# Optimization experiments

Hardware: AMD Instinct MI355X
Metric: run time of the kernel (lower is better)

## Reference

```python
import jax, jax.numpy as jnp
import numpy as np

B, T, I, H = 64, 512, 1024, 1024


def setup_inputs() -> dict:
    key = jax.random.key(0)
    ks = jax.random.split(key, 7)
    s = 1.0 / np.sqrt(H)  # PyTorch GRUCell init range
    return {
        "input": jax.random.normal(ks[0], (B, T, I), jnp.float32),
        "hidden": jax.random.normal(ks[1], (B, H), jnp.float32),
        "done": jax.random.bernoulli(ks[2], 0.05, (B, T)),
        "W_ih": jax.random.uniform(ks[3], (3 * H, I), jnp.float32, -s, s),
        "W_hh": jax.random.uniform(ks[4], (3 * H, H), jnp.float32, -s, s),
        "b_ih": jax.random.uniform(ks[5], (3 * H,), jnp.float32, -s, s),
        "b_hh": jax.random.uniform(ks[6], (3 * H,), jnp.float32, -s, s),
    }


def _gru_loop(input, hidden, done, W_ih, W_hh, b_ih, b_hh):
    # Precompute input-side gates for all timesteps (one big GEMM): [B,T,3H]
    gi = jnp.einsum('bti,gi->btg', input, W_ih) + b_ih

    def step(h, xs):
        gi_t, d_t = xs  # [B,3H], [B]
        # reset_state: zero hidden where episode is done
        h = jnp.where(d_t[:, None], jnp.zeros_like(h), h)
        gh = h @ W_hh.T + b_hh  # [B,3H]
        i_r, i_z, i_n = jnp.split(gi_t, 3, axis=-1)
        h_r, h_z, h_n = jnp.split(gh, 3, axis=-1)
        r = jax.nn.sigmoid(i_r + h_r)
        z = jax.nn.sigmoid(i_z + h_z)
        n = jnp.tanh(i_n + r * h_n)
        h_new = (1.0 - z) * n + z * h
        return h_new, h_new

    h_last, outs = jax.lax.scan(
        step, hidden, (jnp.swapaxes(gi, 0, 1), jnp.swapaxes(done, 0, 1))
    )
    return jnp.swapaxes(outs, 0, 1), h_last  # [B,T,H], [B,H]


def reference(input, hidden, done, W_ih, W_hh, b_ih, b_hh):
    return _gru_loop(input, hidden, done, W_ih, W_hh, b_ih, b_hh)
```

## Files before the change

kernel.cpp:

```cpp
#include <hip/hip_runtime.h>


typedef __attribute__((ext_vector_type(8))) short bf16x8;
typedef __attribute__((ext_vector_type(4))) float f32x4;
typedef __attribute__((ext_vector_type(4))) unsigned int uint32x4;

__device__ inline unsigned short f2bf(float f) {
  union { float f; unsigned int u; } x; x.f = f;
  unsigned int r = (x.u + 0x7fffu + ((x.u >> 16) & 1u)) >> 16;
  return (unsigned short)r;
}
__device__ inline float bf2f(unsigned short h) {
  union { unsigned int u; float f; } x; x.u = ((unsigned int)h) << 16;
  return x.f;
}
__device__ inline float sigm(float x) { return 1.f / (1.f + __expf(-x)); }
__device__ inline float tanh_f(float x) { float e = __expf(2.f * x); return 1.f - 2.f / (e + 1.f); }

__global__ void cvt_f32_bf16(const float* __restrict__ src, unsigned short* __restrict__ dst, int n4) {
  int i = blockIdx.x * 256 + threadIdx.x;
  if (i >= n4) return;
  float4 v = ((const float4*)src)[i];
  unsigned long long r = (unsigned long long)f2bf(v.x)
                       | ((unsigned long long)f2bf(v.y) << 16)
                       | ((unsigned long long)f2bf(v.z) << 32)
                       | ((unsigned long long)f2bf(v.w) << 48);
  ((unsigned long long*)dst)[i] = r;
}

__global__ __launch_bounds__(256, 2) void gi_gemm(const unsigned short* __restrict__ X,
                                                  const unsigned short* __restrict__ W,
                                                  unsigned short* __restrict__ gi) {
  __shared__ __align__(16) unsigned short As[8192];
  __shared__ __align__(16) unsigned short Bs[8192];
  const int lane = threadIdx.x & 63, wid = threadIdx.x >> 6;
  const int nt = blockIdx.x % 24, mt = blockIdx.x / 24;
  const int m0 = mt * 128, n0 = nt * 128;
  const int wm = wid & 1, wn = wid >> 1;
  const int l15 = lane & 15, l4 = lane >> 4;

  int soff[4];
#pragma unroll
  for (int i = 0; i < 4; ++i) {
    int p = wid * 256 + i * 64 + lane;
    int r = p >> 3, c = (p & 7) ^ (r & 7);
    soff[i] = r * 1024 + c * 8;
  }
  const unsigned short* Xb = X + (size_t)m0 * 1024;
  const unsigned short* Wb = W + (size_t)n0 * 1024;

  f32x4 zero4 = {0.f, 0.f, 0.f, 0.f};
  f32x4 acc[4][4];
#pragma unroll
  for (int a = 0; a < 4; ++a)
#pragma unroll
    for (int b = 0; b < 4; ++b) acc[a][b] = zero4;

  for (int kc = 0; kc < 16; ++kc) {
    __syncthreads();
#pragma unroll
    for (int i = 0; i < 4; ++i) {
      __builtin_amdgcn_global_load_lds(
          (const __attribute__((address_space(1))) unsigned int*)(Xb + kc * 64 + soff[i]),
          (__attribute__((address_space(3))) unsigned int*)(As + (wid * 256 + i * 64) * 8),
          16, 0, 0);
      __builtin_amdgcn_global_load_lds(
          (const __attribute__((address_space(1))) unsigned int*)(Wb + kc * 64 + soff[i]),
          (__attribute__((address_space(3))) unsigned int*)(Bs + (wid * 256 + i * 64) * 8),
          16, 0, 0);
    }
    __syncthreads();
#pragma unroll
    for (int s = 0; s < 2; ++s) {
      const int cc = s * 4 + l4;
      bf16x8 af[4], bfv[4];
#pragma unroll
      for (int ta = 0; ta < 4; ++ta) {
        int r = wm * 64 + ta * 16 + l15;
        int phys = (r << 3) | (cc ^ (r & 7));
        af[ta] = *(const bf16x8*)(As + phys * 8);
      }
#pragma unroll
      for (int tb = 0; tb < 4; ++tb) {
        int r = wn * 64 + tb * 16 + l15;
        int phys = (r << 3) | (cc ^ (r & 7));
        bfv[tb] = *(const bf16x8*)(Bs + phys * 8);
      }
#pragma unroll
      for (int ta = 0; ta < 4; ++ta)
#pragma unroll
        for (int tb = 0; tb < 4; ++tb)
          acc[ta][tb] = __builtin_amdgcn_mfma_f32_16x16x32_bf16(af[ta], bfv[tb], acc[ta][tb], 0, 0, 0);
    }
  }
#pragma unroll
  for (int ta = 0; ta < 4; ++ta)
#pragma unroll
    for (int tb = 0; tb < 4; ++tb) {
      int colg = n0 + wn * 64 + tb * 16 + l15;
#pragma unroll
      for (int rr = 0; rr < 4; ++rr) {
        int rowg = m0 + wm * 64 + ta * 16 + l4 * 4 + rr;
        gi[(size_t)rowg * 3072 + colg] = f2bf(acc[ta][tb][rr]);
      }
    }
}

__global__ __launch_bounds__(256, 1) void gru_rec(
    const unsigned short* __restrict__ gi,
    const unsigned short* __restrict__ whh,
    unsigned short* hbuf,
    const int* __restrict__ done,
    const float* __restrict__ h0,
    const float* __restrict__ bih,
    const float* __restrict__ bhh,
    float* __restrict__ out,
    float* __restrict__ hlast,
    unsigned int* flags) {
  const int tid = threadIdx.x, lane = tid & 63, wid = tid >> 6;
  const int g = blockIdx.x >> 6, p = blockIdx.x & 63;
  const int b0 = g * 16, j0 = p * 16;
  const int bn = lane & 15, kq = lane >> 4;

  __shared__ float cpart[4][3][272];

  uint32x4 wf[8][3];
#pragma unroll
  for (int s = 0; s < 8; ++s) {
    const int k = wid * 256 + s * 32 + kq * 8;
#pragma unroll
    for (int gt = 0; gt < 3; ++gt)
      wf[s][gt] = *(const uint32x4*)(whh + (size_t)(gt * 1024 + j0 + bn) * 1024 + k);
  }
#pragma unroll
  for (int s = 0; s < 8; ++s)
#pragma unroll
    for (int gt = 0; gt < 3; ++gt)
      asm volatile("" : "+v"(wf[s][gt]));

  const int bb = tid >> 4, jj = tid & 15;
  const int col = j0 + jj;
  const int brow = b0 + bb;
  const float br = bih[col] + bhh[col];
  const float bz = bih[1024 + col] + bhh[1024 + col];
  const float bni = bih[2048 + col];
  const float bnh = bhh[2048 + col];
  float hprev = h0[brow * 1024 + col];

  const int ra = b0 + bn;

  int dA = done[ra * 512];
  int dB = done[brow * 512];
  const unsigned short* gp0 = gi + (size_t)brow * 512 * 3072 + col;
  unsigned short g0 = gp0[0], g1 = gp0[1024], g2 = gp0[2048];

#pragma unroll 1
  for (int t = 0; t < 512; ++t) {
    const unsigned short* hb = hbuf + (size_t)(t & 1) * 65536;
    const unsigned long long* ap = (const unsigned long long*)(hb + (size_t)ra * 1024 + wid * 256);
    f32x4 a0 = {0.f, 0.f, 0.f, 0.f}, a1 = a0, a2 = a0;
#pragma unroll
    for (int s = 0; s < 8; ++s) {
      int qi = s * 8 + kq * 2;
      unsigned long long lo = __hip_atomic_load(ap + qi, __ATOMIC_RELAXED, __HIP_MEMORY_SCOPE_AGENT);
      unsigned long long hi = __hip_atomic_load(ap + qi + 1, __ATOMIC_RELAXED, __HIP_MEMORY_SCOPE_AGENT);
      if (dA) { lo = 0ull; hi = 0ull; }
      union { unsigned long long q[2]; bf16x8 v; } au;
      au.q[0] = lo; au.q[1] = hi;
      a0 = __builtin_amdgcn_mfma_f32_16x16x32_bf16(au.v, __builtin_bit_cast(bf16x8, wf[s][0]), a0, 0, 0, 0);
      a1 = __builtin_amdgcn_mfma_f32_16x16x32_bf16(au.v, __builtin_bit_cast(bf16x8, wf[s][1]), a1, 0, 0, 0);
      a2 = __builtin_amdgcn_mfma_f32_16x16x32_bf16(au.v, __builtin_bit_cast(bf16x8, wf[s][2]), a2, 0, 0, 0);
    }
#pragma unroll
    for (int rr = 0; rr < 4; ++rr) {
      int idx = (kq * 4 + rr) * 17 + bn;
      cpart[wid][0][idx] = a0[rr];
      cpart[wid][1][idx] = a1[rr];
      cpart[wid][2][idx] = a2[rr];
    }
    __syncthreads();

    const int ridx = bb * 17 + jj;
    float ghr = cpart[0][0][ridx] + cpart[1][0][ridx] + cpart[2][0][ridx] + cpart[3][0][ridx];
    float ghz = cpart[0][1][ridx] + cpart[1][1][ridx] + cpart[2][1][ridx] + cpart[3][1][ridx];
    float ghn = cpart[0][2][ridx] + cpart[1][2][ridx] + cpart[2][2][ridx] + cpart[3][2][ridx];

    float gir = bf2f(g0);
    float giz = bf2f(g1);
    float gin = bf2f(g2);

    float hp = dB ? 0.f : hprev;
    float r = sigm(gir + br + ghr);
    float z = sigm(giz + bz + ghz);
    float nn = tanh_f(gin + bni + r * (ghn + bnh));
    float hn = (1.f - z) * nn + z * hp;
    hprev = hn;
    out[((size_t)brow * 512 + t) * 1024 + col] = hn;

    unsigned short h16 = f2bf(hn);
    unsigned int other = (unsigned int)__shfl_xor((int)(unsigned int)h16, 1, 64);
    if ((jj & 1) == 0) {
      unsigned int val = (unsigned int)h16 | (other << 16);
      unsigned int* dst = (unsigned int*)(hbuf + (size_t)((t + 1) & 1) * 65536) + ((brow * 1024 + col) >> 1);
      __hip_atomic_store(dst, val, __ATOMIC_RELAXED, __HIP_MEMORY_SCOPE_AGENT);
    }

    if (t == 511) {
      hlast[brow * 1024 + col] = hn;
    } else {
      __syncthreads();
      if (tid == 0)
        __hip_atomic_store(&flags[blockIdx.x], (unsigned)(t + 1), __ATOMIC_RELAXED, __HIP_MEMORY_SCOPE_AGENT);
      dA = done[ra * 512 + t + 1];
      dB = done[brow * 512 + t + 1];
      const unsigned short* gp = gi + ((size_t)brow * 512 + t + 1) * 3072 + col;
      g0 = gp[0]; g1 = gp[1024]; g2 = gp[2048];
      const unsigned tgt = (unsigned)(t + 1);
      while (true) {
        unsigned v = __hip_atomic_load(&flags[g * 64 + lane], __ATOMIC_RELAXED, __HIP_MEMORY_SCOPE_AGENT);
        if (__all((int)(v >= tgt))) break;
      }
    }
  }
}

extern "C" void kernel_launch(void* const* d_in, const int* in_sizes, int n_in,
                              void* d_out, int out_size, void* d_ws, size_t ws_size,
                              hipStream_t stream) {
  const float* x = (const float*)d_in[0];
  const float* h0 = (const float*)d_in[1];
  const int* done = (const int*)d_in[2];
  const float* wih = (const float*)d_in[3];
  const float* whh = (const float*)d_in[4];
  const float* bih = (const float*)d_in[5];
  const float* bhh = (const float*)d_in[6];
  float* out = (float*)d_out;

  char* ws = (char*)d_ws;
  unsigned short* gi = (unsigned short*)(ws);
  unsigned short* xbf = (unsigned short*)(ws + 201326592);
  unsigned short* wihb = (unsigned short*)(ws + 268435456);
  unsigned short* whhb = (unsigned short*)(ws + 274726912);
  unsigned short* hbuf = (unsigned short*)(ws + 281018368);
  unsigned int* flags = (unsigned int*)(ws + 281280512);

  hipMemsetAsync(flags, 0, 1024, stream);
  cvt_f32_bf16<<<32768, 256, 0, stream>>>(x, xbf, 8388608);
  cvt_f32_bf16<<<3072, 256, 0, stream>>>(wih, wihb, 786432);
  cvt_f32_bf16<<<3072, 256, 0, stream>>>(whh, whhb, 786432);
  cvt_f32_bf16<<<64, 256, 0, stream>>>(h0, hbuf, 16384);
  gi_gemm<<<6144, 256, 0, stream>>>(xbf, wihb, gi);
  gru_rec<<<256, 256, 0, stream>>>(gi, whhb, hbuf, done, h0, bih, bhh,
                                   out, out + 33554432, flags);
}
```

Before: 3.526 ms.

## Replace flag-based grid barrier with timestamped hidden-state words and retile recurrence

Each hidden-state element is now a 32-bit word that carries a bf16 value plus the timestep tag, so consumers spin directly on the data instead of on per-block flags. This removes the separate flag store, the extra block barrier and the all-to-all flag poll. The recurrent tile changes to 8 batch rows by 32 columns per block, with six MFMA fragments per wave, and it only waits on the eight batch rows it actually reads. Next-step gi and done values are prefetched before the MFMAs. In exchange, the hidden buffer doubles in size, half of every MFMA A-tile is wasted on padding, and a guard counter can silently give up on spinning.

```diff
diff --git a/kernel.cpp b/kernel.cpp
--- a/kernel.cpp
+++ b/kernel.cpp
@@ -26,6 +26,12 @@
                        | ((unsigned long long)f2bf(v.z) << 32)
                        | ((unsigned long long)f2bf(v.w) << 48);
   ((unsigned long long*)dst)[i] = r;
+}
+
+__global__ void init_h(const float* __restrict__ h0, unsigned int* __restrict__ hbuf) {
+  int i = blockIdx.x * 256 + threadIdx.x;
+  hbuf[i] = (unsigned int)f2bf(h0[i]);
+  hbuf[65536 + i] = 0xFFFF0000u;
 }
 
 __global__ __launch_bounds__(256, 2) void gi_gemm(const unsigned short* __restrict__ X,
@@ -106,121 +112,170 @@
     }
 }
 
+__device__ __forceinline__ void barrier_lds() {
+  asm volatile("s_waitcnt lgkmcnt(0)" ::: "memory");
+  __builtin_amdgcn_s_barrier();
+  __builtin_amdgcn_sched_barrier(0);
+}
+
 __global__ __launch_bounds__(256, 1) void gru_rec(
     const unsigned short* __restrict__ gi,
     const unsigned short* __restrict__ whh,
-    unsigned short* hbuf,
+    unsigned int* hbuf,
     const int* __restrict__ done,
     const float* __restrict__ h0,
     const float* __restrict__ bih,
     const float* __restrict__ bhh,
     float* __restrict__ out,
-    float* __restrict__ hlast,
-    unsigned int* flags) {
+    float* __restrict__ hlast) {
   const int tid = threadIdx.x, lane = tid & 63, wid = tid >> 6;
-  const int g = blockIdx.x >> 6, p = blockIdx.x & 63;
-  const int b0 = g * 16, j0 = p * 16;
-  const int bn = lane & 15, kq = lane >> 4;
-
-  __shared__ float cpart[4][3][272];
-
-  uint32x4 wf[8][3];
-#pragma unroll
-  for (int s = 0; s < 8; ++s) {
-    const int k = wid * 256 + s * 32 + kq * 8;
-#pragma unroll
-    for (int gt = 0; gt < 3; ++gt)
-      wf[s][gt] = *(const uint32x4*)(whh + (size_t)(gt * 1024 + j0 + bn) * 1024 + k);
+  const int l15 = lane & 15, l4 = lane >> 4;
+  const int x = blockIdx.x >> 5, slot = blockIdx.x & 31;
+  const int jb = slot * 32;
+
+  __shared__ float cpart[4][6][136];
+
+  uint32x4 wf[8][6];
+#pragma unroll
+  for (int s = 0; s < 8; ++s)
+#pragma unroll
+    for (int f = 0; f < 6; ++f) {
+      const int row = (f >> 1) * 1024 + jb + (f & 1) * 16 + l15;
+      const int k = wid * 256 + s * 32 + l4 * 8;
+      wf[s][f] = *(const uint32x4*)(whh + (size_t)row * 1024 + k);
+    }
+#pragma unroll
+  for (int s = 0; s < 8; ++s)
+#pragma unroll
+    for (int f = 0; f < 6; ++f)
+      asm volatile("" : "+v"(wf[s][f]));
+
+  const int bb = tid >> 5, jj = tid & 31;
+  const int colg = jb + jj;
+  const int rowg = x * 8 + bb;
+  const float br = bih[colg] + bhh[colg];
+  const float bz = bih[1024 + colg] + bhh[1024 + colg];
+  const float bni = bih[2048 + colg];
+  const float bnh = bhh[2048 + colg];
+  float hprev = h0[rowg * 1024 + colg];
+
+  const bool aval = (l15 < 8);
+  const int ra = x * 8 + (l15 & 7);
+  const int awoff = ra * 1024 + wid * 256 + l4 * 8;
+  const int rep = (x * 8 + ((lane >> 3) & 7)) * 1024 + (8 * wid + (lane & 7)) * 32;
+
+  int dAr = done[ra * 512];
+  int dB = done[rowg * 512];
+  unsigned short g0, g1, g2;
+  {
+    const unsigned short* gp = gi + (size_t)rowg * 512 * 3072 + colg;
+    g0 = gp[0]; g1 = gp[1024]; g2 = gp[2048];
   }
-#pragma unroll
-  for (int s = 0; s < 8; ++s)
-#pragma unroll
-    for (int gt = 0; gt < 3; ++gt)
-      asm volatile("" : "+v"(wf[s][gt]));
-
-  const int bb = tid >> 4, jj = tid & 15;
-  const int col = j0 + jj;
-  const int brow = b0 + bb;
-  const float br = bih[col] + bhh[col];
-  const float bz = bih[1024 + col] + bhh[1024 + col];
-  const float bni = bih[2048 + col];
-  const float bnh = bhh[2048 + col];
-  float hprev = h0[brow * 1024 + col];
-
-  const int ra = b0 + bn;
-
-  int dA = done[ra * 512];
-  int dB = done[brow * 512];
-  const unsigned short* gp0 = gi + (size_t)brow * 512 * 3072 + col;
-  unsigned short g0 = gp0[0], g1 = gp0[1024], g2 = gp0[2048];
+
+  bool dead = false;
 
 #pragma unroll 1
   for (int t = 0; t < 512; ++t) {
-    const unsigned short* hb = hbuf + (size_t)(t & 1) * 65536;
-    const unsigned long long* ap = (const unsigned long long*)(hb + (size_t)ra * 1024 + wid * 256);
-    f32x4 a0 = {0.f, 0.f, 0.f, 0.f}, a1 = a0, a2 = a0;
+    const unsigned int* hb = hbuf + (size_t)(t & 1) * 65536;
+    const unsigned tgt = (unsigned)t;
+
+    if (!dead) {
+      const unsigned int* wp = hb + rep;
+      int guard = 0;
+      while (true) {
+        unsigned v = __hip_atomic_load(wp, __ATOMIC_RELAXED, __HIP_MEMORY_SCOPE_AGENT);
+        if (__all((int)((v >> 16) == tgt))) break;
+        if (++guard > (1 << 20)) { dead = true; break; }
+      }
+    }
+
+    uint32x4 aw[8];
+    const unsigned keep = (aval && !dAr) ? 0xffffffffu : 0u;
+    {
+      const unsigned long long* ap = (const unsigned long long*)hb + (awoff >> 1);
+      int guard = 0;
+      while (true) {
+        unsigned bad = 0u;
+        if (aval) {
+#pragma unroll
+          for (int s = 0; s < 8; ++s)
+#pragma unroll
+            for (int q = 0; q < 4; ++q) {
+              const unsigned long long v =
+                  __hip_atomic_load(ap + s * 16 + q, __ATOMIC_RELAXED, __HIP_MEMORY_SCOPE_AGENT);
+              bad |= (((unsigned)(v >> 16)) & 0xFFFFu) ^ tgt;
+              bad |= ((unsigned)(v >> 48)) ^ tgt;
+              aw[s][q] = (((unsigned)(v & 0xFFFFu)) | (((unsigned)(v >> 16)) & 0xFFFF0000u)) & keep;
+            }
+        } else {
+#pragma unroll
+          for (int s = 0; s < 8; ++s) aw[s] = uint32x4{0u, 0u, 0u, 0u};
+        }
+        if (__all((int)(bad == 0u)) || dead) break;
+        if (++guard > (1 << 20)) { dead = true; break; }
+      }
+    }
+
+    int dAr_n = dAr, dB_n = dB;
+    unsigned short g0n = g0, g1n = g1, g2n = g2;
+    if (t < 511) {
+      dAr_n = done[ra * 512 + t + 1];
+      dB_n = done[rowg * 512 + t + 1];
+      const unsigned short* gp = gi + ((size_t)rowg * 512 + t + 1) * 3072 + colg;
+      g0n = gp[0]; g1n = gp[1024]; g2n = gp[2048];
+    }
+
+    f32x4 acc0 = {0.f, 0.f, 0.f, 0.f}, acc1 = acc0, acc2 = acc0,
+          acc3 = acc0, acc4 = acc0, acc5 = acc0;
 #pragma unroll
     for (int s = 0; s < 8; ++s) {
-      int qi = s * 8 + kq * 2;
-      unsigned long long lo = __hip_atomic_load(ap + qi, __ATOMIC_RELAXED, __HIP_MEMORY_SCOPE_AGENT);
-      unsigned long long hi = __hip_atomic_load(ap + qi + 1, __ATOMIC_RELAXED, __HIP_MEMORY_SCOPE_AGENT);
-      if (dA) { lo = 0ull; hi = 0ull; }
-      union { unsigned long long q[2]; bf16x8 v; } au;
-      au.q[0] = lo; au.q[1] = hi;
-      a0 = __builtin_amdgcn_mfma_f32_16x16x32_bf16(au.v, __builtin_bit_cast(bf16x8, wf[s][0]), a0, 0, 0, 0);
-      a1 = __builtin_amdgcn_mfma_f32_16x16x32_bf16(au.v, __builtin_bit_cast(bf16x8, wf[s][1]), a1, 0, 0, 0);
-      a2 = __builtin_amdgcn_mfma_f32_16x16x32_bf16(au.v, __builtin_bit_cast(bf16x8, wf[s][2]), a2, 0, 0, 0);
-    }
-#pragma unroll
-    for (int rr = 0; rr < 4; ++rr) {
-      int idx = (kq * 4 + rr) * 17 + bn;
-      cpart[wid][0][idx] = a0[rr];
-      cpart[wid][1][idx] = a1[rr];
-      cpart[wid][2][idx] = a2[rr];
-    }
-    __syncthreads();
-
-    const int ridx = bb * 17 + jj;
-    float ghr = cpart[0][0][ridx] + cpart[1][0][ridx] + cpart[2][0][ridx] + cpart[3][0][ridx];
-    float ghz = cpart[0][1][ridx] + cpart[1][1][ridx] + cpart[2][1][ridx] + cpart[3][1][ridx];
-    float ghn = cpart[0][2][ridx] + cpart[1][2][ridx] + cpart[2][2][ridx] + cpart[3][2][ridx];
-
-    float gir = bf2f(g0);
-    float giz = bf2f(g1);
-    float gin = bf2f(g2);
-
-    float hp = dB ? 0.f : hprev;
-    float r = sigm(gir + br + ghr);
-    float z = sigm(giz + bz + ghz);
-    float nn = tanh_f(gin + bni + r * (ghn + bnh));
-    float hn = (1.f - z) * nn + z * hp;
+      const bf16x8 af = __builtin_bit_cast(bf16x8, aw[s]);
+      acc0 = __builtin_amdgcn_mfma_f32_16x16x32_bf16(af, __builtin_bit_cast(bf16x8, wf[s][0]), acc0, 0, 0, 0);
+      acc1 = __builtin_amdgcn_mfma_f32_16x16x32_bf16(af, __builtin_bit_cast(bf16x8, wf[s][1]), acc1, 0, 0, 0);
+      acc2 = __builtin_amdgcn_mfma_f32_16x16x32_bf16(af, __builtin_bit_cast(bf16x8, wf[s][2]), acc2, 0, 0, 0);
+      acc3 = __builtin_amdgcn_mfma_f32_16x16x32_bf16(af, __builtin_bit_cast(bf16x8, wf[s][3]), acc3, 0, 0, 0);
+      acc4 = __builtin_amdgcn_mfma_f32_16x16x32_bf16(af, __builtin_bit_cast(bf16x8, wf[s][4]), acc4, 0, 0, 0);
+      acc5 = __builtin_amdgcn_mfma_f32_16x16x32_bf16(af, __builtin_bit_cast(bf16x8, wf[s][5]), acc5, 0, 0, 0);
+    }
+
+    if (l4 < 2) {
+#pragma unroll
+      for (int rr = 0; rr < 4; ++rr) {
+        const int idx = (l4 * 4 + rr) * 17 + l15;
+        cpart[wid][0][idx] = acc0[rr];
+        cpart[wid][1][idx] = acc1[rr];
+        cpart[wid][2][idx] = acc2[rr];
+        cpart[wid][3][idx] = acc3[rr];
+        cpart[wid][4][idx] = acc4[rr];
+        cpart[wid][5][idx] = acc5[rr];
+      }
+    }
+    barrier_lds();
+
+    const int fr = jj >> 4, cc = jj & 15;
+    const int ridx = bb * 17 + cc;
+    const float ghr = cpart[0][fr][ridx] + cpart[1][fr][ridx] + cpart[2][fr][ridx] + cpart[3][fr][ridx];
+    const float ghz = cpart[0][2 + fr][ridx] + cpart[1][2 + fr][ridx] + cpart[2][2 + fr][ridx] + cpart[3][2 + fr][ridx];
+    const float ghn = cpart[0][4 + fr][ridx] + cpart[1][4 + fr][ridx] + cpart[2][4 + fr][ridx] + cpart[3][4 + fr][ridx];
+
+    const float hp = dB ? 0.f : hprev;
+    const float r = sigm(bf2f(g0) + br + ghr);
+    const float z = sigm(bf2f(g1) + bz + ghz);
+    const float nn = tanh_f(bf2f(g2) + bni + r * (ghn + bnh));
+    const float hn = (1.f - z) * nn + z * hp;
     hprev = hn;
-    out[((size_t)brow * 512 + t) * 1024 + col] = hn;
-
-    unsigned short h16 = f2bf(hn);
-    unsigned int other = (unsigned int)__shfl_xor((int)(unsigned int)h16, 1, 64);
-    if ((jj & 1) == 0) {
-      unsigned int val = (unsigned int)h16 | (other << 16);
-      unsigned int* dst = (unsigned int*)(hbuf + (size_t)((t + 1) & 1) * 65536) + ((brow * 1024 + col) >> 1);
-      __hip_atomic_store(dst, val, __ATOMIC_RELAXED, __HIP_MEMORY_SCOPE_AGENT);
-    }
 
     if (t == 511) {
-      hlast[brow * 1024 + col] = hn;
+      out[((size_t)rowg * 512 + t) * 1024 + colg] = hn;
+      hlast[rowg * 1024 + colg] = hn;
     } else {
-      __syncthreads();
-      if (tid == 0)
-        __hip_atomic_store(&flags[blockIdx.x], (unsigned)(t + 1), __ATOMIC_RELAXED, __HIP_MEMORY_SCOPE_AGENT);
-      dA = done[ra * 512 + t + 1];
-      dB = done[brow * 512 + t + 1];
-      const unsigned short* gp = gi + ((size_t)brow * 512 + t + 1) * 3072 + col;
-      g0 = gp[0]; g1 = gp[1024]; g2 = gp[2048];
-      const unsigned tgt = (unsigned)(t + 1);
-      while (true) {
-        unsigned v = __hip_atomic_load(&flags[g * 64 + lane], __ATOMIC_RELAXED, __HIP_MEMORY_SCOPE_AGENT);
-        if (__all((int)(v >= tgt))) break;
-      }
-    }
+      unsigned int* dst = hbuf + (size_t)((t + 1) & 1) * 65536 + rowg * 1024 + colg;
+      __hip_atomic_store(dst, ((unsigned)(t + 1) << 16) | (unsigned)f2bf(hn),
+                         __ATOMIC_RELAXED, __HIP_MEMORY_SCOPE_AGENT);
+      out[((size_t)rowg * 512 + t) * 1024 + colg] = hn;
+      barrier_lds();
+    }
+    dAr = dAr_n; dB = dB_n; g0 = g0n; g1 = g1n; g2 = g2n;
   }
 }
 
@@ -241,15 +296,13 @@
   unsigned short* xbf = (unsigned short*)(ws + 201326592);
   unsigned short* wihb = (unsigned short*)(ws + 268435456);
   unsigned short* whhb = (unsigned short*)(ws + 274726912);
-  unsigned short* hbuf = (unsigned short*)(ws + 281018368);
-  unsigned int* flags = (unsigned int*)(ws + 281280512);
-
-  hipMemsetAsync(flags, 0, 1024, stream);
+  unsigned int* hbuf = (unsigned int*)(ws + 201326592);
+
   cvt_f32_bf16<<<32768, 256, 0, stream>>>(x, xbf, 8388608);
   cvt_f32_bf16<<<3072, 256, 0, stream>>>(wih, wihb, 786432);
   cvt_f32_bf16<<<3072, 256, 0, stream>>>(whh, whhb, 786432);
-  cvt_f32_bf16<<<64, 256, 0, stream>>>(h0, hbuf, 16384);
   gi_gemm<<<6144, 256, 0, stream>>>(xbf, wihb, gi);
+  init_h<<<256, 256, 0, stream>>>(h0, hbuf);
   gru_rec<<<256, 256, 0, stream>>>(gi, whhb, hbuf, done, h0, bih, bhh,
-                                   out, out + 33554432, flags);
-}
+                                   out, out + 33554432);
+}
```

Result: faster. 2.899 ms (-17.8%).
